# Kernel tuning notes

Hardware: AMD Instinct MI355X
Metric: run time of the kernel (lower is better)

Reference implementation:

```python
import jax, jax.numpy as jnp
import numpy as np

B, TQ, TK, D, DV = 8, 2048, 2048, 1024, 1024  # units == TK


def setup_inputs() -> dict:
    key = jax.random.key(0)
    kq, kk, kv, kb = jax.random.split(key, 4)
    q = jax.random.normal(kq, (B, TQ, D), dtype=jnp.float32)
    k = jax.random.normal(kk, (B, D, TK), dtype=jnp.float32)
    v = jax.random.normal(kv, (B, TK, DV), dtype=jnp.float32)
    b = 0.1 * jax.random.normal(kb, (TK,), dtype=jnp.float32)  # bias over key axis (units,)
    return {"q": q, "k": k, "v": v, "b": b}


def reference(q, k, v, b):
    # scores[b,i,j] = tanh(q_i . k_j + b_j)   -- additive-style biased dot scores
    scores = jnp.tanh(jnp.einsum("bqd,bdk->bqk", q, k) + b)  # [B, TQ, TK]
    # softmax over the key axis (axis=1 of the unbatched [TQ,TK] scores)
    weights = jax.nn.softmax(scores, axis=-1)
    # weighted sum of values
    context = jnp.einsum("bqk,bkv->bqv", weights, v)  # [B, TQ, DV]
    return context
```

## Files before the change

kernel.cpp:

```cpp
#include <hip/hip_runtime.h>
#include <hip/hip_bf16.h>
#include <stdint.h>

#define B_  8
#define TQ_ 2048
#define TK_ 2048
#define D_  1024
#define DV_ 1024

typedef __attribute__((ext_vector_type(8))) short  short8;
typedef __attribute__((ext_vector_type(4))) float  floatx4;

__device__ __forceinline__ void async_copy16(const void* g, void* l) {
  __builtin_amdgcn_global_load_lds(
      (const __attribute__((address_space(1))) unsigned int*)g,
      (__attribute__((address_space(3))) unsigned int*)l,
      16, 0, 0);
}

__device__ __forceinline__ ushort f2bf(float f) {
  union { __hip_bfloat16 b; ushort u; } cv;
  cv.b = __float2bfloat16(f);
  return cv.u;
}

__device__ __forceinline__ float bf2f(ushort u) {
  union { ushort u; __hip_bfloat16 b; } cv;
  cv.u = u;
  return __bfloat162float(cv.b);
}


__global__ void cvt_bf16(const float4* __restrict__ in, ushort4* __restrict__ out, int n4) {
  int i = blockIdx.x * 256 + threadIdx.x;
  if (i < n4) {
    float4 f = in[i];
    ushort4 o;
    o.x = f2bf(f.x); o.y = f2bf(f.y); o.z = f2bf(f.z); o.w = f2bf(f.w);
    out[i] = o;
  }
}

__global__ void transpose_cvt(const float* __restrict__ in, ushort* __restrict__ out,
                              int R, int C) {
  __shared__ float tile[32][33];
  int tx = threadIdx.x, ty = threadIdx.y;
  int c0 = blockIdx.x * 32, r0 = blockIdx.y * 32;
  size_t zoff = (size_t)blockIdx.z * R * C;
  #pragma unroll
  for (int i = 0; i < 4; i++)
    tile[ty + i * 8][tx] = in[zoff + (size_t)(r0 + ty + i * 8) * C + (c0 + tx)];
  __syncthreads();
  #pragma unroll
  for (int i = 0; i < 4; i++)
    out[zoff + (size_t)(c0 + ty + i * 8) * R + (r0 + tx)] = f2bf(tile[tx][ty + i * 8]);
}

template <int KDIM>
__device__ __forceinline__ void gemm_core(const ushort* __restrict__ Ab,
                                          const ushort* __restrict__ Bb,
                                          ushort* ldsA, ushort* ldsB,
                                          int bm0, int bn0,
                                          floatx4 (&acc)[4][4]) {
  const int t    = threadIdx.x;
  const int lane = t & 63;
  const int w    = t >> 6;
  const int wm   = w >> 1, wn = w & 1;
  const int lc   = lane & 15;
  const int kg   = (lane >> 4) * 16;

  const char* ga0 = (const char*)(Ab + (size_t)(bm0 + (t >> 2)) * KDIM) + (t & 3) * 16;
  const char* ga1 = ga0 + (size_t)64 * KDIM * 2;
  const char* gb0 = (const char*)(Bb + (size_t)(bn0 + (t >> 2)) * KDIM) + (t & 3) * 16;
  const char* gb1 = gb0 + (size_t)64 * KDIM * 2;
  char* la0 = (char*)ldsA + t * 16;
  char* la1 = (char*)ldsA + 4096 + t * 16;
  char* lb0 = (char*)ldsB + t * 16;
  char* lb1 = (char*)ldsB + 4096 + t * 16;

  const char* afp[4];
  const char* bfp[4];
  #pragma unroll
  for (int i = 0; i < 4; i++) {
    afp[i] = (const char*)ldsA + (wm * 64 + i * 16 + lc) * 64 + kg;
    bfp[i] = (const char*)ldsB + (wn * 64 + i * 16 + lc) * 64 + kg;
  }

  #pragma unroll
  for (int mi = 0; mi < 4; mi++)
    #pragma unroll
    for (int ni = 0; ni < 4; ni++)
      acc[mi][ni] = (floatx4){0.f, 0.f, 0.f, 0.f};

  for (int k0 = 0; k0 < KDIM; k0 += 32) {
    __syncthreads();
    async_copy16(ga0, la0);
    async_copy16(ga1, la1);
    async_copy16(gb0, lb0);
    async_copy16(gb1, lb1);
    ga0 += 64; ga1 += 64; gb0 += 64; gb1 += 64;
    __syncthreads();

    short8 af[4], bfr[4];
    #pragma unroll
    for (int i = 0; i < 4; i++) af[i] = *(const short8*)(afp[i]);
    #pragma unroll
    for (int i = 0; i < 4; i++) bfr[i] = *(const short8*)(bfp[i]);
    #pragma unroll
    for (int mi = 0; mi < 4; mi++)
      #pragma unroll
      for (int ni = 0; ni < 4; ni++)
        acc[mi][ni] = __builtin_amdgcn_mfma_f32_16x16x32_bf16(af[mi], bfr[ni],
                                                              acc[mi][ni], 0, 0, 0);
  }
}

__global__ void gemm_qk(const ushort* __restrict__ Q, const ushort* __restrict__ Kt,
                        const float* __restrict__ bias, ushort* __restrict__ P,
                        float* __restrict__ lsum) {
  __shared__ ushort ldsA[128 * 32];
  __shared__ ushort ldsB[128 * 32];
  const int z   = blockIdx.z;
  const int bm0 = blockIdx.y * 128;
  const int bn0 = blockIdx.x * 128;

  floatx4 acc[4][4];
  gemm_core<D_>(Q + (size_t)z * TQ_ * D_, Kt + (size_t)z * TK_ * D_,
                ldsA, ldsB, bm0, bn0, acc);

  const int lane = threadIdx.x & 63;
  const int w    = threadIdx.x >> 6;
  const int wm   = w >> 1, wn = w & 1;
  const int lc   = lane & 15;
  ushort* Pb = P + (size_t)z * TQ_ * TK_;
  float*  lz = lsum + z * TQ_;

  #pragma unroll
  for (int mi = 0; mi < 4; mi++) {
    int grow = bm0 + wm * 64 + mi * 16 + ((lane >> 4) << 2);
    float rs[4] = {0.f, 0.f, 0.f, 0.f};
    #pragma unroll
    for (int ni = 0; ni < 4; ni++) {
      int gcol = bn0 + wn * 64 + ni * 16 + lc;
      float bj = bias[gcol];
      #pragma unroll
      for (int r = 0; r < 4; r++) {
        float s = acc[mi][ni][r] + bj;
        float tnh = 1.f - 2.f / (__expf(2.f * s) + 1.f);
        float p   = __expf(tnh);
        ushort pu = f2bf(p);
        Pb[(size_t)(grow + r) * TK_ + gcol] = pu;
        rs[r] += bf2f(pu);
      }
    }
    #pragma unroll
    for (int r = 0; r < 4; r++) {
      rs[r] += __shfl_xor(rs[r], 1, 64);
      rs[r] += __shfl_xor(rs[r], 2, 64);
      rs[r] += __shfl_xor(rs[r], 4, 64);
      rs[r] += __shfl_xor(rs[r], 8, 64);
    }
    if (lc == 0) {
      #pragma unroll
      for (int r = 0; r < 4; r++) atomicAdd(&lz[grow + r], rs[r]);
    }
  }
}

__global__ void gemm_pv(const ushort* __restrict__ P, const ushort* __restrict__ Vt,
                        const float* __restrict__ lsum, float* __restrict__ out) {
  __shared__ ushort ldsA[128 * 32];
  __shared__ ushort ldsB[128 * 32];
  const int z   = blockIdx.z;
  const int bm0 = blockIdx.y * 128;
  const int bn0 = blockIdx.x * 128;

  floatx4 acc[4][4];
  gemm_core<TK_>(P + (size_t)z * TQ_ * TK_, Vt + (size_t)z * DV_ * TK_,
                 ldsA, ldsB, bm0, bn0, acc);

  const int lane = threadIdx.x & 63;
  const int w    = threadIdx.x >> 6;
  const int wm   = w >> 1, wn = w & 1;
  const int lc   = lane & 15;
  float* ob = out + (size_t)z * TQ_ * DV_;
  const float* lz = lsum + z * TQ_;

  #pragma unroll
  for (int mi = 0; mi < 4; mi++) {
    int grow = bm0 + wm * 64 + mi * 16 + ((lane >> 4) << 2);
    float linv[4];
    #pragma unroll
    for (int r = 0; r < 4; r++) linv[r] = 1.f / lz[grow + r];
    #pragma unroll
    for (int ni = 0; ni < 4; ni++) {
      int gcol = bn0 + wn * 64 + ni * 16 + lc;
      #pragma unroll
      for (int r = 0; r < 4; r++)
        ob[(size_t)(grow + r) * DV_ + gcol] = acc[mi][ni][r] * linv[r];
    }
  }
}


extern "C" void kernel_launch(void* const* d_in, const int* in_sizes, int n_in,
                              void* d_out, int out_size, void* d_ws, size_t ws_size,
                              hipStream_t stream) {
  const float* q    = (const float*)d_in[0];
  const float* k    = (const float*)d_in[1];
  const float* v    = (const float*)d_in[2];
  const float* bias = (const float*)d_in[3];
  float* out = (float*)d_out;

  char* ws = (char*)d_ws;
  ushort* qb   = (ushort*)(ws);
  ushort* ktb  = (ushort*)(ws + 33554432);
  ushort* vtb  = (ushort*)(ws + 67108864);
  ushort* P    = (ushort*)(ws + 100663296);
  float*  lsum = (float*)(ws + 167772160);

  hipMemsetAsync(lsum, 0, B_ * TQ_ * sizeof(float), stream);

  int n4q = B_ * TQ_ * D_ / 4;
  cvt_bf16<<<dim3(n4q / 256), dim3(256), 0, stream>>>((const float4*)q, (ushort4*)qb, n4q);
  transpose_cvt<<<dim3(TK_ / 32, D_ / 32, B_), dim3(32, 8), 0, stream>>>(k, ktb, D_, TK_);
  transpose_cvt<<<dim3(DV_ / 32, TK_ / 32, B_), dim3(32, 8), 0, stream>>>(v, vtb, TK_, DV_);

  gemm_qk<<<dim3(TK_ / 128, TQ_ / 128, B_), dim3(256), 0, stream>>>(qb, ktb, bias, P, lsum);
  gemm_pv<<<dim3(DV_ / 128, TQ_ / 128, B_), dim3(256), 0, stream>>>(P, vtb, lsum, out);
}
```

Measured before the change: 417.1 us.

## Double GEMM K-tile to 64 with XOR-swizzled LDS and vectorized 64x64 transpose

The shared GEMM core now stages a 64-wide K slice per iteration instead of 32. Global rows are loaded with an XOR chunk swizzle so the MFMA fragment reads from LDS avoid bank conflicts. This halves the number of barrier pairs per output tile, at the cost of doubling LDS per block. The transpose-convert kernels for K and V are replaced by a 64x64 tiled version using float4 loads and ushort4 stores to cut memory transactions.

```diff
diff --git a/kernel.cpp b/kernel.cpp
--- a/kernel.cpp
+++ b/kernel.cpp
@@ -41,19 +41,37 @@
   }
 }
 
-__global__ void transpose_cvt(const float* __restrict__ in, ushort* __restrict__ out,
-                              int R, int C) {
-  __shared__ float tile[32][33];
-  int tx = threadIdx.x, ty = threadIdx.y;
-  int c0 = blockIdx.x * 32, r0 = blockIdx.y * 32;
-  size_t zoff = (size_t)blockIdx.z * R * C;
-  #pragma unroll
-  for (int i = 0; i < 4; i++)
-    tile[ty + i * 8][tx] = in[zoff + (size_t)(r0 + ty + i * 8) * C + (c0 + tx)];
+__global__ void transpose_cvt64(const float* __restrict__ in, ushort* __restrict__ out,
+                                int R, int C) {
+  __shared__ float tile[64][65];
+  const int t  = threadIdx.x;
+  const int c0 = blockIdx.x * 64, r0 = blockIdx.y * 64;
+  const size_t z = (size_t)blockIdx.z * R * C;
+  {
+    const int row = t >> 4, col = (t & 15) * 4;
+    #pragma unroll
+    for (int ro = 0; ro < 4; ro++) {
+      const float4 f = *(const float4*)&in[z + (size_t)(r0 + ro * 16 + row) * C + c0 + col];
+      tile[ro * 16 + row][col + 0] = f.x;
+      tile[ro * 16 + row][col + 1] = f.y;
+      tile[ro * 16 + row][col + 2] = f.z;
+      tile[ro * 16 + row][col + 3] = f.w;
+    }
+  }
   __syncthreads();
-  #pragma unroll
-  for (int i = 0; i < 4; i++)
-    out[zoff + (size_t)(c0 + ty + i * 8) * R + (r0 + tx)] = f2bf(tile[tx][ty + i * 8]);
+  {
+    const int c = t >> 4, rg = (t & 15) * 4;
+    #pragma unroll
+    for (int ro = 0; ro < 4; ro++) {
+      const int cc = ro * 16 + c;
+      ushort4 o;
+      o.x = f2bf(tile[rg + 0][cc]);
+      o.y = f2bf(tile[rg + 1][cc]);
+      o.z = f2bf(tile[rg + 2][cc]);
+      o.w = f2bf(tile[rg + 3][cc]);
+      *(ushort4*)&out[z + (size_t)(c0 + cc) * R + r0 + rg] = o;
+    }
+  }
 }
 
 template <int KDIM>
@@ -67,24 +85,26 @@
   const int w    = t >> 6;
   const int wm   = w >> 1, wn = w & 1;
   const int lc   = lane & 15;
-  const int kg   = (lane >> 4) * 16;
-
-  const char* ga0 = (const char*)(Ab + (size_t)(bm0 + (t >> 2)) * KDIM) + (t & 3) * 16;
-  const char* ga1 = ga0 + (size_t)64 * KDIM * 2;
-  const char* gb0 = (const char*)(Bb + (size_t)(bn0 + (t >> 2)) * KDIM) + (t & 3) * 16;
-  const char* gb1 = gb0 + (size_t)64 * KDIM * 2;
-  char* la0 = (char*)ldsA + t * 16;
-  char* la1 = (char*)ldsA + 4096 + t * 16;
-  char* lb0 = (char*)ldsB + t * 16;
-  char* lb1 = (char*)ldsB + 4096 + t * 16;
-
-  const char* afp[4];
-  const char* bfp[4];
-  #pragma unroll
-  for (int i = 0; i < 4; i++) {
-    afp[i] = (const char*)ldsA + (wm * 64 + i * 16 + lc) * 64 + kg;
-    bfp[i] = (const char*)ldsB + (wn * 64 + i * 16 + lc) * 64 + kg;
-  }
+  const int q    = lane >> 4;
+
+  const int arow   = t >> 3;
+  const int achunk = (t & 7) ^ (arow & 7);
+  const char* gA[4];
+  const char* gB[4];
+  char* lA[4];
+  char* lB[4];
+  #pragma unroll
+  for (int ro = 0; ro < 4; ro++) {
+    gA[ro] = (const char*)(Ab + (size_t)(bm0 + ro * 32 + arow) * KDIM) + achunk * 16;
+    gB[ro] = (const char*)(Bb + (size_t)(bn0 + ro * 32 + arow) * KDIM) + achunk * 16;
+    lA[ro] = (char*)ldsA + (ro * 256 + t) * 16;
+    lB[ro] = (char*)ldsB + (ro * 256 + t) * 16;
+  }
+
+  const int baseA0 = (wm * 64 + lc) * 128 + ((q    ) ^ (lc & 7)) * 16;
+  const int baseA1 = (wm * 64 + lc) * 128 + ((q + 4) ^ (lc & 7)) * 16;
+  const int baseB0 = (wn * 64 + lc) * 128 + ((q    ) ^ (lc & 7)) * 16;
+  const int baseB1 = (wn * 64 + lc) * 128 + ((q + 4) ^ (lc & 7)) * 16;
 
   #pragma unroll
   for (int mi = 0; mi < 4; mi++)
@@ -92,34 +112,43 @@
     for (int ni = 0; ni < 4; ni++)
       acc[mi][ni] = (floatx4){0.f, 0.f, 0.f, 0.f};
 
-  for (int k0 = 0; k0 < KDIM; k0 += 32) {
+  for (int k0 = 0; k0 < KDIM; k0 += 64) {
     __syncthreads();
-    async_copy16(ga0, la0);
-    async_copy16(ga1, la1);
-    async_copy16(gb0, lb0);
-    async_copy16(gb1, lb1);
-    ga0 += 64; ga1 += 64; gb0 += 64; gb1 += 64;
+    #pragma unroll
+    for (int ro = 0; ro < 4; ro++) { async_copy16(gA[ro], lA[ro]); gA[ro] += 128; }
+    #pragma unroll
+    for (int ro = 0; ro < 4; ro++) { async_copy16(gB[ro], lB[ro]); gB[ro] += 128; }
     __syncthreads();
 
     short8 af[4], bfr[4];
     #pragma unroll
-    for (int i = 0; i < 4; i++) af[i] = *(const short8*)(afp[i]);
-    #pragma unroll
-    for (int i = 0; i < 4; i++) bfr[i] = *(const short8*)(bfp[i]);
+    for (int i = 0; i < 4; i++) af[i]  = *(const short8*)((const char*)ldsA + baseA0 + i * 2048);
+    #pragma unroll
+    for (int i = 0; i < 4; i++) bfr[i] = *(const short8*)((const char*)ldsB + baseB0 + i * 2048);
     #pragma unroll
     for (int mi = 0; mi < 4; mi++)
       #pragma unroll
       for (int ni = 0; ni < 4; ni++)
         acc[mi][ni] = __builtin_amdgcn_mfma_f32_16x16x32_bf16(af[mi], bfr[ni],
                                                               acc[mi][ni], 0, 0, 0);
+    #pragma unroll
+    for (int i = 0; i < 4; i++) af[i]  = *(const short8*)((const char*)ldsA + baseA1 + i * 2048);
+    #pragma unroll
+    for (int i = 0; i < 4; i++) bfr[i] = *(const short8*)((const char*)ldsB + baseB1 + i * 2048);
+    #pragma unroll
+    for (int mi = 0; mi < 4; mi++)
+      #pragma unroll
+      for (int ni = 0; ni < 4; ni++)
+        acc[mi][ni] = __builtin_amdgcn_mfma_f32_16x16x32_bf16(af[mi], bfr[ni],
+                                                              acc[mi][ni], 0, 0, 0);
   }
 }
 
 __global__ void gemm_qk(const ushort* __restrict__ Q, const ushort* __restrict__ Kt,
                         const float* __restrict__ bias, ushort* __restrict__ P,
                         float* __restrict__ lsum) {
-  __shared__ ushort ldsA[128 * 32];
-  __shared__ ushort ldsB[128 * 32];
+  __shared__ ushort ldsA[128 * 64];
+  __shared__ ushort ldsB[128 * 64];
   const int z   = blockIdx.z;
   const int bm0 = blockIdx.y * 128;
   const int bn0 = blockIdx.x * 128;
@@ -169,8 +198,8 @@
 
 __global__ void gemm_pv(const ushort* __restrict__ P, const ushort* __restrict__ Vt,
                         const float* __restrict__ lsum, float* __restrict__ out) {
-  __shared__ ushort ldsA[128 * 32];
-  __shared__ ushort ldsB[128 * 32];
+  __shared__ ushort ldsA[128 * 64];
+  __shared__ ushort ldsB[128 * 64];
   const int z   = blockIdx.z;
   const int bm0 = blockIdx.y * 128;
   const int bn0 = blockIdx.x * 128;
@@ -223,8 +252,8 @@
 
   int n4q = B_ * TQ_ * D_ / 4;
   cvt_bf16<<<dim3(n4q / 256), dim3(256), 0, stream>>>((const float4*)q, (ushort4*)qb, n4q);
-  transpose_cvt<<<dim3(TK_ / 32, D_ / 32, B_), dim3(32, 8), 0, stream>>>(k, ktb, D_, TK_);
-  transpose_cvt<<<dim3(DV_ / 32, TK_ / 32, B_), dim3(32, 8), 0, stream>>>(v, vtb, TK_, DV_);
+  transpose_cvt64<<<dim3(TK_ / 64, D_ / 64, B_), dim3(256), 0, stream>>>(k, ktb, D_, TK_);
+  transpose_cvt64<<<dim3(DV_ / 64, TK_ / 64, B_), dim3(256), 0, stream>>>(v, vtb, TK_, DV_);
 
   gemm_qk<<<dim3(TK_ / 128, TQ_ / 128, B_), dim3(256), 0, stream>>>(qb, ktb, bias, P, lsum);
   gemm_pv<<<dim3(DV_ / 128, TQ_ / 128, B_), dim3(256), 0, stream>>>(P, vtb, lsum, out);
```

New measurement: 554.0 us. 32.8% more time.
